# Kernel tuning notes

Measured on AMD Instinct MI355X. Metric: run time of the kernel, lower is better.

## Reference

```python
import jax, jax.numpy as jnp
import numpy as np

# Faithful reference for NeighborSample: the original builds a one-hot
# input[y+i-2, x+j-2, k] into output channel s = k*25 + i*5 + j, then
# reshapes [b,h,w,c,5,5] -> transpose -> [b*h*w,5,5,c].
# Equivalently: zero-pad by 2 and gather every 5x5 neighborhood per pixel.

def setup_inputs() -> dict:
    key = jax.random.key(0)
    x = jax.random.normal(key, (8, 64, 64, 192), dtype=jnp.float32)
    return {"x": x}


def reference(x) -> jnp.ndarray:
    b, h, w, c = x.shape
    K = 5  # neighborhood size
    pad = K // 2
    xp = jnp.pad(x, ((0, 0), (pad, pad), (pad, pad), (0, 0)))  # zero pad == conv SAME
    # 25 shifted views stacked on a new axis -> [b, h, w, 25, c]
    patches = jnp.stack(
        [xp[:, i:i + h, j:j + w, :] for i in range(K) for j in range(K)],
        axis=3,
    )
    # [b, h, w, 25, c] -> [b*h*w, 5, 5, c]
    return patches.reshape(b * h * w, K, K, c)
```

## Files before the change

kernel.cpp:

```cpp
#include <hip/hip_runtime.h>


constexpr int B = 8;
constexpr int H = 64;
constexpr int W = 64;
constexpr int C = 192;
constexpr int C4 = C / 4;
constexpr int K = 5;
constexpr int PAD = K / 2;

constexpr unsigned TOTAL_F4 = (unsigned)B * H * W * K * K * C4;
constexpr int BLOCK = 256;

__global__ __launch_bounds__(BLOCK) void neighbor_sample_kernel(
    const float4* __restrict__ in, float4* __restrict__ out) {
  unsigned gid = blockIdx.x * BLOCK + threadIdx.x;

  unsigned k4   = gid % C4;
  unsigned rest = gid / C4;
  unsigned pos  = rest % (K * K);
  unsigned p    = rest / (K * K);

  int i = (int)(pos / K);
  int j = (int)(pos % K);

  int xx = (int)(p & (W - 1));
  int yy = (int)((p >> 6) & (H - 1));
  int b  = (int)(p >> 12);

  int sy = yy + i - PAD;
  int sx = xx + j - PAD;

  float4 v = make_float4(0.f, 0.f, 0.f, 0.f);
  if ((unsigned)sy < (unsigned)H && (unsigned)sx < (unsigned)W) {
    unsigned src = (((unsigned)(b * H + sy) * W) + (unsigned)sx) * C4 + k4;
    v = in[src];
  }
  out[gid] = v;
}

extern "C" void kernel_launch(void* const* d_in, const int* in_sizes, int n_in,
                              void* d_out, int out_size, void* d_ws, size_t ws_size,
                              hipStream_t stream) {
  const float4* in = (const float4*)d_in[0];
  float4* out = (float4*)d_out;
  unsigned grid = TOTAL_F4 / BLOCK;
  neighbor_sample_kernel<<<grid, BLOCK, 0, stream>>>(in, out);
}
```

Measured before the change: 659.4 us.

## Replace per-output gather with per-input scatter to 25 neighbor slots

```diff
diff --git a/kernel.cpp b/kernel.cpp
--- a/kernel.cpp
+++ b/kernel.cpp
@@ -1,49 +1,64 @@
 #include <hip/hip_runtime.h>
 
+
+typedef float f32x4 __attribute__((ext_vector_type(4)));
 
 constexpr int B = 8;
 constexpr int H = 64;
 constexpr int W = 64;
-constexpr int C = 192;
-constexpr int C4 = C / 4;
+constexpr int C4 = 48;
 constexpr int K = 5;
 constexpr int PAD = K / 2;
+constexpr int ROW = K * K * C4;
 
-constexpr unsigned TOTAL_F4 = (unsigned)B * H * W * K * K * C4;
+constexpr unsigned NPIX  = (unsigned)B * H * W;
+constexpr unsigned TOTAL = NPIX * C4;
 constexpr int BLOCK = 256;
+constexpr unsigned GRID = TOTAL / BLOCK;
 
-__global__ __launch_bounds__(BLOCK) void neighbor_sample_kernel(
-    const float4* __restrict__ in, float4* __restrict__ out) {
-  unsigned gid = blockIdx.x * BLOCK + threadIdx.x;
-
-  unsigned k4   = gid % C4;
-  unsigned rest = gid / C4;
-  unsigned pos  = rest % (K * K);
-  unsigned p    = rest / (K * K);
-
-  int i = (int)(pos / K);
-  int j = (int)(pos % K);
+__global__ __launch_bounds__(BLOCK) void neighbor_scatter_kernel(
+    const f32x4* __restrict__ in, f32x4* __restrict__ out) {
+  unsigned g  = blockIdx.x * BLOCK + threadIdx.x;
+  unsigned k4 = g % C4;
+  unsigned p  = g / C4;
 
   int xx = (int)(p & (W - 1));
   int yy = (int)((p >> 6) & (H - 1));
-  int b  = (int)(p >> 12);
 
-  int sy = yy + i - PAD;
-  int sx = xx + j - PAD;
+  f32x4 v = in[g];
+  int pbase = (int)(p * (unsigned)ROW + k4);
 
-  float4 v = make_float4(0.f, 0.f, 0.f, 0.f);
-  if ((unsigned)sy < (unsigned)H && (unsigned)sx < (unsigned)W) {
-    unsigned src = (((unsigned)(b * H + sy) * W) + (unsigned)sx) * C4 + k4;
-    v = in[src];
+  bool interior = (yy >= PAD) & (yy < H - PAD) & (xx >= PAD) & (xx < W - PAD);
+
+  if (__all(interior)) {
+#pragma unroll
+    for (int oi = 0; oi < K; ++oi)
+#pragma unroll
+      for (int oj = 0; oj < K; ++oj) {
+        const int off = ((PAD - oi) * W + (PAD - oj)) * ROW + (oi * K + oj) * C4;
+        out[pbase + off] = v;
+      }
+  } else {
+    const f32x4 z = {0.f, 0.f, 0.f, 0.f};
+#pragma unroll
+    for (int oi = 0; oi < K; ++oi)
+#pragma unroll
+      for (int oj = 0; oj < K; ++oj) {
+        const int off = ((PAD - oi) * W + (PAD - oj)) * ROW + (oi * K + oj) * C4;
+        int ty = yy + PAD - oi, tx = xx + PAD - oj;
+        if ((unsigned)ty < (unsigned)H && (unsigned)tx < (unsigned)W)
+          out[pbase + off] = v;
+        int sy = yy + oi - PAD, sx = xx + oj - PAD;
+        if (!((unsigned)sy < (unsigned)H && (unsigned)sx < (unsigned)W))
+          out[pbase + (oi * K + oj) * C4] = z;
+      }
   }
-  out[gid] = v;
 }
 
 extern "C" void kernel_launch(void* const* d_in, const int* in_sizes, int n_in,
                               void* d_out, int out_size, void* d_ws, size_t ws_size,
                               hipStream_t stream) {
-  const float4* in = (const float4*)d_in[0];
-  float4* out = (float4*)d_out;
-  unsigned grid = TOTAL_F4 / BLOCK;
-  neighbor_sample_kernel<<<grid, BLOCK, 0, stream>>>(in, out);
+  const f32x4* in = (const f32x4*)d_in[0];
+  f32x4* out = (f32x4*)d_out;
+  neighbor_scatter_kernel<<<GRID, BLOCK, 0, stream>>>(in, out);
 }
```

After: 629.6 us. 4.5% less time.
